# Performance work log

Hardware: AMD Instinct MI355X
Metric: run time of the kernel (lower is better)

The kernel has to match this reference:

```python
import jax, jax.numpy as jnp
import numpy as np

B = 16384
D_IN = 1024
D_OUT = 512
H1 = 4 * D_IN      # floor(layersDimentions[0]*inputDimention) = 4096
H3 = 4 * D_OUT     # floor(layersDimentions[1]*outputDimention) = 2048
H4 = 4 * D_OUT     # floor(layersDimentions[2]*outputDimention) = 2048
M = 256            # codebook size


def _linear_params(key, fan_in, fan_out):
    kw, kb = jax.random.split(key)
    bound = 1.0 / np.sqrt(fan_in)
    w = jax.random.uniform(kw, (fan_out, fan_in), jnp.float32, -bound, bound)
    b = jax.random.uniform(kb, (fan_out,), jnp.float32, -bound, bound)
    return w, b


def setup_inputs() -> dict:
    key = jax.random.key(0)
    ks = jax.random.split(key, 7)
    x = jax.random.normal(ks[0], (B, D_IN), jnp.float32)
    codebook = jnp.sort(jax.random.normal(ks[1], (M,), jnp.float32))
    w1, b1 = _linear_params(ks[2], D_IN, H1)
    w2, b2 = _linear_params(ks[3], H1, D_OUT)
    w3, b3 = _linear_params(ks[4], D_OUT, H3)
    w4, b4 = _linear_params(ks[5], H3, H4)
    w5, b5 = _linear_params(ks[6], H4, D_OUT)
    return {"x": x, "codebook": codebook,
            "w1": w1, "b1": b1, "w2": w2, "b2": b2,
            "w3": w3, "b3": b3, "w4": w4, "b4": b4,
            "w5": w5, "b5": b5}


def _quantize(x, codebook):
    # nearest codeword per scalar element: argmin_m |x - c_m|
    # x: [B, D], codebook: [M]
    d = jnp.abs(x[..., None] - codebook)          # [B, D, M]
    idx = jnp.argmin(d, axis=-1)                  # [B, D]
    return codebook[idx]


def reference(x, codebook, w1, b1, w2, b2, w3, b3, w4, b4, w5, b5):
    h = x @ w1.T + b1                # [B, H1]
    h = h @ w2.T + b2                # [B, D_OUT]
    h = _quantize(h, codebook)       # [B, D_OUT]
    h = h @ w3.T + b3                # [B, H3]
    h = h @ w4.T + b4                # [B, H4]
    return h @ w5.T + b5             # [B, D_OUT]
```

## Files before the change

### kernel.cpp

```cpp
#include <hip/hip_runtime.h>


typedef __bf16 v8bf __attribute__((ext_vector_type(8)));
typedef float  v4f  __attribute__((ext_vector_type(4)));

#define Bdim   16384
#define DIN    1024
#define DOUT   512
#define H1dim  4096
#define H3dim  2048
#define H4dim  2048

#define GLOBAL_AS __attribute__((address_space(1)))
#define LDS_AS    __attribute__((address_space(3)))

__device__ __forceinline__ void load16_to_lds(const __bf16* g, __bf16* l) {
  __builtin_amdgcn_global_load_lds((const GLOBAL_AS unsigned int*)g,
                                   (LDS_AS unsigned int*)l, 16, 0, 0);
}

__device__ __forceinline__ unsigned pack2bf(float a, float b) {
  return (unsigned)__builtin_bit_cast(unsigned short, (__bf16)a) |
         ((unsigned)__builtin_bit_cast(unsigned short, (__bf16)b) << 16);
}

__device__ __forceinline__ void transpose_body(const float* __restrict__ in,
                                               __bf16* __restrict__ out,
                                               int R, int C, int bx, int by,
                                               float (*tile)[68]) {
  const int c0 = bx * 32, r0 = by * 64;
  const int t = threadIdx.x, tr = t >> 5, tc = t & 31;
#pragma unroll
  for (int i = 0; i < 8; ++i)
    tile[tc][tr + i * 8] = in[(size_t)(r0 + tr + i * 8) * C + (c0 + tc)];
  __syncthreads();
  const int orow = t >> 3, oc = (t & 7) * 8;
  float4 a = *(const float4*)&tile[orow][oc];
  float4 b = *(const float4*)&tile[orow][oc + 4];
  int4 o;
  o.x = pack2bf(a.x, a.y); o.y = pack2bf(a.z, a.w);
  o.z = pack2bf(b.x, b.y); o.w = pack2bf(b.z, b.w);
  *(int4*)&out[(size_t)(c0 + orow) * R + (r0 + oc)] = o;
}

__device__ __forceinline__ void cast_body(const float* __restrict__ in,
                                          __bf16* __restrict__ out, int b) {
  const size_t i = (size_t)b * 2048 + (size_t)threadIdx.x * 8;
  float4 a = *(const float4*)&in[i];
  float4 c = *(const float4*)&in[i + 4];
  int4 o;
  o.x = pack2bf(a.x, a.y); o.y = pack2bf(a.z, a.w);
  o.z = pack2bf(c.x, c.y); o.w = pack2bf(c.z, c.w);
  *(int4*)&out[i] = o;
}

__global__ void prep_kernel(const float* __restrict__ w1, __bf16* __restrict__ w1T,
                            const float* __restrict__ w4, __bf16* __restrict__ w4T,
                            const float* __restrict__ w3, __bf16* __restrict__ w3T,
                            const float* __restrict__ x, __bf16* __restrict__ xb,
                            const float* __restrict__ w2, __bf16* __restrict__ w2b,
                            const float* __restrict__ w5, __bf16* __restrict__ w5b) {
  __shared__ float tile[32][68];
  int b = blockIdx.x;
  if (b < 2048) {
    transpose_body(w1, w1T, H1dim, DIN, b & 31, b >> 5, tile);
  } else if (b < 4096) {
    b -= 2048;
    transpose_body(w4, w4T, H4dim, H3dim, b & 63, b >> 6, tile);
  } else if (b < 4608) {
    b -= 4096;
    transpose_body(w3, w3T, H3dim, DOUT, b & 15, b >> 4, tile);
  } else if (b < 12800) {
    cast_body(x, xb, b - 4608);
  } else if (b < 13824) {
    cast_body(w2, w2b, b - 12800);
  } else {
    cast_body(w5, w5b, b - 13824);
  }
}

__device__ __forceinline__ void bias_ba_body(int bb, const float* __restrict__ b1,
                                             const float* __restrict__ w2,
                                             const float* __restrict__ b2,
                                             float* __restrict__ ba) {
  const int wave = threadIdx.x >> 6, lane = threadIdx.x & 63;
  const int j = bb * 4 + wave;
  float s = 0.f;
  for (int k = lane; k < H1dim; k += 64) s += b1[k] * w2[(size_t)j * H1dim + k];
#pragma unroll
  for (int off = 32; off; off >>= 1) s += __shfl_xor(s, off, 64);
  if (lane == 0) ba[j] = s + b2[j];
}

__device__ __forceinline__ void bias_bc_body(int bb, const float* __restrict__ b3,
                                             const __bf16* __restrict__ WtT,
                                             const float* __restrict__ b4,
                                             const float* __restrict__ w5,
                                             const float* __restrict__ b5,
                                             float* __restrict__ bc) {
  const int wave = threadIdx.x >> 6, lane = threadIdx.x & 63;
  const int j = bb * 4 + wave;
  float s = 0.f;
  for (int k = lane; k < H4dim; k += 64)
    s += b3[k] * (float)WtT[(size_t)j * H4dim + k] + b4[k] * w5[(size_t)j * H4dim + k];
#pragma unroll
  for (int off = 32; off; off >>= 1) s += __shfl_xor(s, off, 64);
  if (lane == 0) bc[j] = s + b5[j];
}

enum { MODE_W = 0, MODE_Q = 1, MODE_OUT = 2 };

#define ASM_BAR() asm volatile("s_barrier" ::: "memory")

template <int MODE, int BM>
__device__ __forceinline__ void gemm_body(__bf16* As, __bf16* Bs, float* cbs,
                                          int bx, int by,
                                          const __bf16* __restrict__ A,
                                          const __bf16* __restrict__ Bt,
                                          void* __restrict__ Cout,
                                          const float* __restrict__ bias,
                                          const float* __restrict__ codebook,
                                          int M, int N, int K, int CH) {
  const int t = threadIdx.x;
  const int m0 = bx * BM, n0 = by * 64;
  if constexpr (MODE == MODE_Q) cbs[t] = codebook[t];

  const int lane = t & 63, wave = t >> 6;
  const int quad = lane >> 4, l15 = lane & 15;
  constexpr int MI = BM / 32;
  const int wm = (wave & 1) * (BM / 2), wn = (wave >> 1) * 32;

  const int lrow = lane >> 3;
  const int gcol = ((lane & 7) ^ lrow) * 8;
  const __bf16* gA = A  + (size_t)(m0 + (BM / 4) * wave + lrow) * K + gcol;
  const __bf16* gB = Bt + (size_t)(n0 + 16 * wave + lrow) * K + gcol;
  const int swz = l15 & 7;

  v4f acc[MI][2], accT[MI][2];
#pragma unroll
  for (int i = 0; i < MI; ++i)
#pragma unroll
    for (int j = 0; j < 2; ++j) {
      acc[i][j] = (v4f){0.f, 0.f, 0.f, 0.f};
      if constexpr (MODE == MODE_W) accT[i][j] = (v4f){0.f, 0.f, 0.f, 0.f};
    }

  auto stage = [&](int k0, int buf) {
    __bf16* lA = As + buf * (BM * 64) + (BM / 4) * wave * 64;
    __bf16* lB = Bs + buf * (64 * 64) + 16 * wave * 64;
#pragma unroll
    for (int p = 0; p < MI; ++p)
      load16_to_lds(gA + (size_t)(8 * p) * K + k0, lA + p * 512);
#pragma unroll
    for (int p = 0; p < 2; ++p)
      load16_to_lds(gB + (size_t)(8 * p) * K + k0, lB + p * 512);
  };

  const int nk = K >> 6;
  const int chsteps = CH >> 6;
  stage(0, 0);
  stage(64, 1);

  int cc = 0;
  for (int tk = 0; tk < nk; ++tk) {
    if (tk + 1 < nk) {
      if constexpr (BM == 128) asm volatile("s_waitcnt vmcnt(6)" ::: "memory");
      else                     asm volatile("s_waitcnt vmcnt(4)" ::: "memory");
    } else {
      asm volatile("s_waitcnt vmcnt(0)" ::: "memory");
    }
    ASM_BAR();

    const __bf16* cA = As + (tk & 1) * (BM * 64);
    const __bf16* cB = Bs + (tk & 1) * (64 * 64);
#pragma unroll
    for (int kk = 0; kk < 2; ++kk) {
      const int cch = ((kk * 4 + quad) ^ swz) * 8;
      v8bf af[MI], bv[2];
#pragma unroll
      for (int i = 0; i < MI; ++i)
        af[i] = *(const v8bf*)&cA[(wm + i * 16 + l15) * 64 + cch];
#pragma unroll
      for (int j = 0; j < 2; ++j)
        bv[j] = *(const v8bf*)&cB[(wn + j * 16 + l15) * 64 + cch];
#pragma unroll
      for (int i = 0; i < MI; ++i)
#pragma unroll
        for (int j = 0; j < 2; ++j)
          acc[i][j] = __builtin_amdgcn_mfma_f32_16x16x32_bf16(af[i], bv[j], acc[i][j], 0, 0, 0);
    }
    if constexpr (MODE == MODE_W) {
      if (++cc == chsteps) {
        cc = 0;
#pragma unroll
        for (int i = 0; i < MI; ++i)
#pragma unroll
          for (int j = 0; j < 2; ++j) {
            accT[i][j] += acc[i][j];
            acc[i][j] = (v4f){0.f, 0.f, 0.f, 0.f};
          }
      }
    }
    asm volatile("s_waitcnt lgkmcnt(0)" ::: "memory");
    ASM_BAR();
    if (tk + 2 < nk) stage((tk + 2) << 6, tk & 1);
  }

#pragma unroll
  for (int j = 0; j < 2; ++j) {
    const int gn = n0 + wn + j * 16 + l15;
    float bj = 0.f;
    if constexpr (MODE != MODE_W) bj = bias[gn];
#pragma unroll
    for (int i = 0; i < MI; ++i) {
#pragma unroll
      for (int r = 0; r < 4; ++r) {
        const int gm = m0 + wm + i * 16 + quad * 4 + r;
        if constexpr (MODE == MODE_W) {
          ((__bf16*)Cout)[(size_t)gm * N + gn] = (__bf16)accT[i][j][r];
        } else if constexpr (MODE == MODE_Q) {
          float v = acc[i][j][r] + bj;
          int idx = 0;
#pragma unroll
          for (int s = 128; s > 0; s >>= 1) {
            const int u = idx + s;
            if (cbs[u] <= v) idx = u;
          }
          float best = cbs[idx];
          if (idx < 255) {
            const float c1 = cbs[idx + 1];
            if (!(v - best <= c1 - v)) best = c1;
          }
          ((__bf16*)Cout)[(size_t)gm * N + gn] = (__bf16)best;
        } else {
          ((float*)Cout)[(size_t)gm * N + gn] = acc[i][j][r] + bj;
        }
      }
    }
  }
}

__global__ __launch_bounds__(256, 3)
void foldA_kernel(const __bf16* __restrict__ w2b, const __bf16* __restrict__ w1T,
                  __bf16* __restrict__ WaT,
                  const __bf16* __restrict__ w5b, const __bf16* __restrict__ w4T,
                  __bf16* __restrict__ WtT,
                  const float* __restrict__ b1, const float* __restrict__ w2,
                  const float* __restrict__ b2, float* __restrict__ ba) {
  __shared__ __align__(16) __bf16 As[2 * 64 * 64];
  __shared__ __align__(16) __bf16 Bs[2 * 64 * 64];
  int b = blockIdx.x;
  if (b < 128) {
    const int c = b & 7, i = b >> 3;
    gemm_body<MODE_W, 64>(As, Bs, nullptr, i >> 1, c * 2 + (i & 1), w2b, w1T, WaT,
                          nullptr, nullptr, DOUT, DIN, H1dim, 512);
  } else if (b < 384) {
    b -= 128;
    const int c = b & 7, i = b >> 3;
    gemm_body<MODE_W, 64>(As, Bs, nullptr, i >> 2, c * 4 + (i & 3), w5b, w4T, WtT,
                          nullptr, nullptr, DOUT, H3dim, H4dim, 512);
  } else {
    bias_ba_body(b - 384, b1, w2, b2, ba);
  }
}

__global__ __launch_bounds__(256, 3)
void foldB_kernel(const __bf16* __restrict__ WtT, const __bf16* __restrict__ w3T,
                  __bf16* __restrict__ WcT,
                  const float* __restrict__ b3, const float* __restrict__ b4,
                  const float* __restrict__ w5, const float* __restrict__ b5,
                  float* __restrict__ bc,
                  const __bf16* __restrict__ xb, const __bf16* __restrict__ WaT,
                  __bf16* __restrict__ q, const float* __restrict__ ba,
                  const float* __restrict__ cb) {
  __shared__ __align__(16) __bf16 As[2 * 128 * 64];
  __shared__ __align__(16) __bf16 Bs[2 * 64 * 64];
  __shared__ float cbs[256];
  int b = blockIdx.x;
  if (b < 64) {
    const int c = b & 7, i = b >> 3;
    gemm_body<MODE_W, 64>(As, Bs, nullptr, i, c, WtT, w3T, WcT,
                          nullptr, nullptr, DOUT, DOUT, H3dim, 256);
  } else if (b < 192) {
    bias_bc_body(b - 64, b3, WtT, b4, w5, b5, bc);
  } else {
    b -= 192;
    const int c = b & 7, i = b >> 3;
    gemm_body<MODE_Q, 128>(As, Bs, cbs, c * 16 + (i >> 3), i & 7, xb, WaT, q,
                           ba, cb, Bdim, DOUT, DIN, DIN);
  }
}

__global__ __launch_bounds__(256, 3)
void gemmout_kernel(const __bf16* __restrict__ q, const __bf16* __restrict__ WcT,
                    float* __restrict__ out, const float* __restrict__ bc) {
  __shared__ __align__(16) __bf16 As[2 * 128 * 64];
  __shared__ __align__(16) __bf16 Bs[2 * 64 * 64];
  const int b = blockIdx.x;
  const int c = b & 7, i = b >> 3;
  gemm_body<MODE_OUT, 128>(As, Bs, nullptr, c * 16 + (i >> 3), i & 7,
                           q, WcT, out, bc, nullptr, Bdim, DOUT, DOUT, DOUT);
}

extern "C" void kernel_launch(void* const* d_in, const int* in_sizes, int n_in,
                              void* d_out, int out_size, void* d_ws, size_t ws_size,
                              hipStream_t stream) {
  const float* x  = (const float*)d_in[0];
  const float* cb = (const float*)d_in[1];
  const float* w1 = (const float*)d_in[2];
  const float* b1 = (const float*)d_in[3];
  const float* w2 = (const float*)d_in[4];
  const float* b2 = (const float*)d_in[5];
  const float* w3 = (const float*)d_in[6];
  const float* b3 = (const float*)d_in[7];
  const float* w4 = (const float*)d_in[8];
  const float* b4 = (const float*)d_in[9];
  const float* w5 = (const float*)d_in[10];
  const float* b5 = (const float*)d_in[11];
  float* out = (float*)d_out;

  char* ws = (char*)d_ws;
  size_t off = 0;
  auto alloc = [&](size_t bytes) -> void* {
    void* p = ws + off;
    off = (off + bytes + 255) & ~(size_t)255;
    return p;
  };
  __bf16* w1T = (__bf16*)alloc((size_t)DIN * H1dim * 2);
  __bf16* w4T = (__bf16*)alloc((size_t)H3dim * H4dim * 2);
  __bf16* w3T = (__bf16*)alloc((size_t)DOUT * H3dim * 2);
  __bf16* w2b = (__bf16*)alloc((size_t)DOUT * H1dim * 2);
  __bf16* w5b = (__bf16*)alloc((size_t)DOUT * H4dim * 2);
  __bf16* WaT = (__bf16*)alloc((size_t)DOUT * DIN * 2);
  __bf16* WtT = (__bf16*)alloc((size_t)DOUT * H3dim * 2);
  __bf16* WcT = (__bf16*)alloc((size_t)DOUT * DOUT * 2);
  __bf16* q   = (__bf16*)alloc((size_t)Bdim * DOUT * 2);
  __bf16* xb  = (__bf16*)alloc((size_t)Bdim * DIN * 2);
  float*  ba  = (float*)alloc(DOUT * 4);
  float*  bc  = (float*)alloc(DOUT * 4);

  prep_kernel<<<14336, 256, 0, stream>>>(w1, w1T, w4, w4T, w3, w3T,
                                         x, xb, w2, w2b, w5, w5b);

  foldA_kernel<<<512, 256, 0, stream>>>(w2b, w1T, WaT, w5b, w4T, WtT,
                                        b1, w2, b2, ba);

  foldB_kernel<<<1216, 256, 0, stream>>>(WtT, w3T, WcT, b3, b4, w5, b5, bc,
                                         xb, WaT, q, ba, cb);

  gemmout_kernel<<<1024, 256, 0, stream>>>(q, WcT, out, bc);
}
```

Before: 268.0 us.

## Fuse quantize GEMM and output GEMM into one kernel with LDS-resident q tile

Replaces the separate quantize-GEMM (x·Wa + codebook snap) and output GEMM with a single kernel. Each block computes a 64-row by 512-column tile, quantizes it into shared memory, then multiplies it by WcT directly, so the q intermediate never goes to global memory. The fold work for WcT and bc moves into its own small kernel, because it can no longer share a launch with the q GEMM. In exchange the fused kernel launches only 256 blocks at one block per CU with a large LDS footprint. It also holds 64 accumulator vectors per thread and reloads WcT for every block without double-buffering in the second phase, which risks lower occupancy and poorer latency hiding.

```diff
diff --git a/kernel.cpp b/kernel.cpp
--- a/kernel.cpp
+++ b/kernel.cpp
@@ -108,23 +108,19 @@
   if (lane == 0) bc[j] = s + b5[j];
 }
 
-enum { MODE_W = 0, MODE_Q = 1, MODE_OUT = 2 };
+enum { MODE_W = 0 };
 
 #define ASM_BAR() asm volatile("s_barrier" ::: "memory")
 
 template <int MODE, int BM>
-__device__ __forceinline__ void gemm_body(__bf16* As, __bf16* Bs, float* cbs,
+__device__ __forceinline__ void gemm_body(__bf16* As, __bf16* Bs,
                                           int bx, int by,
                                           const __bf16* __restrict__ A,
                                           const __bf16* __restrict__ Bt,
                                           void* __restrict__ Cout,
-                                          const float* __restrict__ bias,
-                                          const float* __restrict__ codebook,
                                           int M, int N, int K, int CH) {
   const int t = threadIdx.x;
   const int m0 = bx * BM, n0 = by * 64;
-  if constexpr (MODE == MODE_Q) cbs[t] = codebook[t];
-
   const int lane = t & 63, wave = t >> 6;
   const int quad = lane >> 4, l15 = lane & 15;
   constexpr int MI = BM / 32;
@@ -142,7 +138,7 @@
 #pragma unroll
     for (int j = 0; j < 2; ++j) {
       acc[i][j] = (v4f){0.f, 0.f, 0.f, 0.f};
-      if constexpr (MODE == MODE_W) accT[i][j] = (v4f){0.f, 0.f, 0.f, 0.f};
+      accT[i][j] = (v4f){0.f, 0.f, 0.f, 0.f};
     }
 
   auto stage = [&](int k0, int buf) {
@@ -163,12 +159,8 @@
 
   int cc = 0;
   for (int tk = 0; tk < nk; ++tk) {
-    if (tk + 1 < nk) {
-      if constexpr (BM == 128) asm volatile("s_waitcnt vmcnt(6)" ::: "memory");
-      else                     asm volatile("s_waitcnt vmcnt(4)" ::: "memory");
-    } else {
-      asm volatile("s_waitcnt vmcnt(0)" ::: "memory");
-    }
+    if (tk + 1 < nk) asm volatile("s_waitcnt vmcnt(4)" ::: "memory");
+    else             asm volatile("s_waitcnt vmcnt(0)" ::: "memory");
     ASM_BAR();
 
     const __bf16* cA = As + (tk & 1) * (BM * 64);
@@ -189,17 +181,15 @@
         for (int j = 0; j < 2; ++j)
           acc[i][j] = __builtin_amdgcn_mfma_f32_16x16x32_bf16(af[i], bv[j], acc[i][j], 0, 0, 0);
     }
-    if constexpr (MODE == MODE_W) {
-      if (++cc == chsteps) {
-        cc = 0;
-#pragma unroll
-        for (int i = 0; i < MI; ++i)
-#pragma unroll
-          for (int j = 0; j < 2; ++j) {
-            accT[i][j] += acc[i][j];
-            acc[i][j] = (v4f){0.f, 0.f, 0.f, 0.f};
-          }
-      }
+    if (++cc == chsteps) {
+      cc = 0;
+#pragma unroll
+      for (int i = 0; i < MI; ++i)
+#pragma unroll
+        for (int j = 0; j < 2; ++j) {
+          accT[i][j] += acc[i][j];
+          acc[i][j] = (v4f){0.f, 0.f, 0.f, 0.f};
+        }
     }
     asm volatile("s_waitcnt lgkmcnt(0)" ::: "memory");
     ASM_BAR();
@@ -209,34 +199,13 @@
 #pragma unroll
   for (int j = 0; j < 2; ++j) {
     const int gn = n0 + wn + j * 16 + l15;
-    float bj = 0.f;
-    if constexpr (MODE != MODE_W) bj = bias[gn];
-#pragma unroll
-    for (int i = 0; i < MI; ++i) {
-#pragma unroll
-      for (int r = 0; r < 4; ++r) {
-        const int gm = m0 + wm + i * 16 + quad * 4 + r;
-        if constexpr (MODE == MODE_W) {
-          ((__bf16*)Cout)[(size_t)gm * N + gn] = (__bf16)accT[i][j][r];
-        } else if constexpr (MODE == MODE_Q) {
-          float v = acc[i][j][r] + bj;
-          int idx = 0;
-#pragma unroll
-          for (int s = 128; s > 0; s >>= 1) {
-            const int u = idx + s;
-            if (cbs[u] <= v) idx = u;
-          }
-          float best = cbs[idx];
-          if (idx < 255) {
-            const float c1 = cbs[idx + 1];
-            if (!(v - best <= c1 - v)) best = c1;
-          }
-          ((__bf16*)Cout)[(size_t)gm * N + gn] = (__bf16)best;
-        } else {
-          ((float*)Cout)[(size_t)gm * N + gn] = acc[i][j][r] + bj;
-        }
+#pragma unroll
+    for (int i = 0; i < MI; ++i)
+#pragma unroll
+      for (int r2 = 0; r2 < 4; ++r2) {
+        const int gm = m0 + wm + i * 16 + quad * 4 + r2;
+        ((__bf16*)Cout)[(size_t)gm * N + gn] = (__bf16)accT[i][j][r2];
       }
-    }
   }
 }
 
@@ -252,54 +221,177 @@
   int b = blockIdx.x;
   if (b < 128) {
     const int c = b & 7, i = b >> 3;
-    gemm_body<MODE_W, 64>(As, Bs, nullptr, i >> 1, c * 2 + (i & 1), w2b, w1T, WaT,
-                          nullptr, nullptr, DOUT, DIN, H1dim, 512);
+    gemm_body<MODE_W, 64>(As, Bs, i >> 1, c * 2 + (i & 1), w2b, w1T, WaT,
+                          DOUT, DIN, H1dim, 512);
   } else if (b < 384) {
     b -= 128;
     const int c = b & 7, i = b >> 3;
-    gemm_body<MODE_W, 64>(As, Bs, nullptr, i >> 2, c * 4 + (i & 3), w5b, w4T, WtT,
-                          nullptr, nullptr, DOUT, H3dim, H4dim, 512);
+    gemm_body<MODE_W, 64>(As, Bs, i >> 2, c * 4 + (i & 3), w5b, w4T, WtT,
+                          DOUT, H3dim, H4dim, 512);
   } else {
     bias_ba_body(b - 384, b1, w2, b2, ba);
   }
 }
 
 __global__ __launch_bounds__(256, 3)
-void foldB_kernel(const __bf16* __restrict__ WtT, const __bf16* __restrict__ w3T,
-                  __bf16* __restrict__ WcT,
-                  const float* __restrict__ b3, const float* __restrict__ b4,
-                  const float* __restrict__ w5, const float* __restrict__ b5,
-                  float* __restrict__ bc,
-                  const __bf16* __restrict__ xb, const __bf16* __restrict__ WaT,
-                  __bf16* __restrict__ q, const float* __restrict__ ba,
-                  const float* __restrict__ cb) {
-  __shared__ __align__(16) __bf16 As[2 * 128 * 64];
+void foldB2_kernel(const __bf16* __restrict__ WtT, const __bf16* __restrict__ w3T,
+                   __bf16* __restrict__ WcT,
+                   const float* __restrict__ b3, const float* __restrict__ b4,
+                   const float* __restrict__ w5, const float* __restrict__ b5,
+                   float* __restrict__ bc) {
+  __shared__ __align__(16) __bf16 As[2 * 64 * 64];
   __shared__ __align__(16) __bf16 Bs[2 * 64 * 64];
-  __shared__ float cbs[256];
   int b = blockIdx.x;
   if (b < 64) {
     const int c = b & 7, i = b >> 3;
-    gemm_body<MODE_W, 64>(As, Bs, nullptr, i, c, WtT, w3T, WcT,
-                          nullptr, nullptr, DOUT, DOUT, H3dim, 256);
-  } else if (b < 192) {
+    gemm_body<MODE_W, 64>(As, Bs, i, c, WtT, w3T, WcT, DOUT, DOUT, H3dim, 256);
+  } else {
     bias_bc_body(b - 64, b3, WtT, b4, w5, b5, bc);
-  } else {
-    b -= 192;
-    const int c = b & 7, i = b >> 3;
-    gemm_body<MODE_Q, 128>(As, Bs, cbs, c * 16 + (i >> 3), i & 7, xb, WaT, q,
-                           ba, cb, Bdim, DOUT, DIN, DIN);
-  }
-}
-
-__global__ __launch_bounds__(256, 3)
-void gemmout_kernel(const __bf16* __restrict__ q, const __bf16* __restrict__ WcT,
-                    float* __restrict__ out, const float* __restrict__ bc) {
-  __shared__ __align__(16) __bf16 As[2 * 128 * 64];
-  __shared__ __align__(16) __bf16 Bs[2 * 64 * 64];
-  const int b = blockIdx.x;
-  const int c = b & 7, i = b >> 3;
-  gemm_body<MODE_OUT, 128>(As, Bs, nullptr, c * 16 + (i >> 3), i & 7,
-                           q, WcT, out, bc, nullptr, Bdim, DOUT, DOUT, DOUT);
+  }
+}
+
+__global__ __launch_bounds__(256, 1)
+void fused_qo_kernel(const __bf16* __restrict__ xb, const __bf16* __restrict__ WaT,
+                     const __bf16* __restrict__ WcT,
+                     const float* __restrict__ ba, const float* __restrict__ bc,
+                     const float* __restrict__ cb, float* __restrict__ out) {
+  __shared__ __align__(16) __bf16 qs[64 * 512];
+  __shared__ __align__(16) __bf16 Bb[2 * 512 * 32];
+  __shared__ __align__(16) __bf16 Ab[2 * 64 * 32];
+  __shared__ float cbs[256];
+
+  const int t = threadIdx.x, lane = t & 63, wave = t >> 6;
+  const int quad = lane >> 4, l15 = lane & 15;
+  const int m0 = blockIdx.x * 64;
+  cbs[t] = cb[t];
+
+  const int wm = (wave & 1) * 32, wn = (wave >> 1) * 32;
+
+  const int scol = ((lane & 3) ^ ((lane >> 3) & 3)) * 8;
+  const __bf16* gA = xb  + (size_t)(m0 + 16 * wave + (lane >> 2)) * 1024 + scol;
+  const __bf16* gB = WaT + (size_t)(128 * wave + (lane >> 2)) * 1024 + scol;
+
+  auto stage1 = [&](int k0, int buf) {
+    load16_to_lds(gA + k0, Ab + buf * 2048 + wave * 512);
+#pragma unroll
+    for (int p = 0; p < 8; ++p)
+      load16_to_lds(gB + (size_t)p * 16384 + k0, Bb + buf * 16384 + wave * 4096 + p * 512);
+  };
+
+  v4f acc[8][2][2];
+#pragma unroll
+  for (int jn = 0; jn < 8; ++jn)
+#pragma unroll
+    for (int i = 0; i < 2; ++i)
+#pragma unroll
+      for (int j = 0; j < 2; ++j) acc[jn][i][j] = (v4f){0.f, 0.f, 0.f, 0.f};
+
+  stage1(0, 0);
+  stage1(32, 1);
+
+  const int rk = (l15 >> 1) & 3;
+  for (int ks = 0; ks < 32; ++ks) {
+    if (ks + 1 < 32) asm volatile("s_waitcnt vmcnt(9)" ::: "memory");
+    else             asm volatile("s_waitcnt vmcnt(0)" ::: "memory");
+    ASM_BAR();
+
+    const __bf16* cA = Ab + (ks & 1) * 2048;
+    const __bf16* cB = Bb + (ks & 1) * 16384;
+    const int cch = (quad ^ rk) * 8;
+    v8bf af0 = *(const v8bf*)&cA[(wm +  0 + l15) * 32 + cch];
+    v8bf af1 = *(const v8bf*)&cA[(wm + 16 + l15) * 32 + cch];
+#pragma unroll
+    for (int jn = 0; jn < 8; ++jn) {
+      v8bf bv0 = *(const v8bf*)&cB[(jn * 64 + wn +  0 + l15) * 32 + cch];
+      v8bf bv1 = *(const v8bf*)&cB[(jn * 64 + wn + 16 + l15) * 32 + cch];
+      acc[jn][0][0] = __builtin_amdgcn_mfma_f32_16x16x32_bf16(af0, bv0, acc[jn][0][0], 0, 0, 0);
+      acc[jn][1][0] = __builtin_amdgcn_mfma_f32_16x16x32_bf16(af1, bv0, acc[jn][1][0], 0, 0, 0);
+      acc[jn][0][1] = __builtin_amdgcn_mfma_f32_16x16x32_bf16(af0, bv1, acc[jn][0][1], 0, 0, 0);
+      acc[jn][1][1] = __builtin_amdgcn_mfma_f32_16x16x32_bf16(af1, bv1, acc[jn][1][1], 0, 0, 0);
+    }
+    asm volatile("s_waitcnt lgkmcnt(0)" ::: "memory");
+    ASM_BAR();
+    if (ks + 2 < 32) stage1((ks + 2) * 32, ks & 1);
+  }
+
+#pragma unroll
+  for (int jn = 0; jn < 8; ++jn) {
+#pragma unroll
+    for (int j = 0; j < 2; ++j) {
+      const int cc = wn + j * 16 + l15;
+      const float bj = ba[jn * 64 + cc];
+#pragma unroll
+      for (int i = 0; i < 2; ++i) {
+#pragma unroll
+        for (int r = 0; r < 4; ++r) {
+          const int row = wm + i * 16 + quad * 4 + r;
+          float v = acc[jn][i][j][r] + bj;
+          int idx = 0;
+#pragma unroll
+          for (int s = 128; s > 0; s >>= 1) {
+            const int u = idx + s;
+            if (cbs[u] <= v) idx = u;
+          }
+          float best = cbs[idx];
+          if (idx < 255) {
+            const float c1 = cbs[idx + 1];
+            if (!(v - best <= c1 - v)) best = c1;
+          }
+          qs[row * 512 + jn * 64 + (((cc >> 3) ^ (row & 7)) * 8) + (cc & 7)] = (__bf16)best;
+        }
+      }
+    }
+  }
+  asm volatile("s_waitcnt lgkmcnt(0)" ::: "memory");
+  ASM_BAR();
+
+#pragma unroll 1
+  for (int jn2 = 0; jn2 < 8; ++jn2) {
+    const int n02 = jn2 * 64;
+#pragma unroll
+    for (int p = 0; p < 16; ++p) {
+      const int row = 16 * wave + p;
+      const int g = (lane >> 3) * 64 + (((lane & 7) ^ (p & 7)) * 8);
+      load16_to_lds(WcT + (size_t)(n02 + row) * 512 + g, Bb + row * 512);
+    }
+    asm volatile("s_waitcnt vmcnt(0)" ::: "memory");
+    ASM_BAR();
+
+    v4f a2[2][2];
+#pragma unroll
+    for (int i = 0; i < 2; ++i)
+#pragma unroll
+      for (int j = 0; j < 2; ++j) a2[i][j] = (v4f){0.f, 0.f, 0.f, 0.f};
+
+#pragma unroll
+    for (int kt = 0; kt < 8; ++kt) {
+#pragma unroll
+      for (int kk = 0; kk < 2; ++kk) {
+        const int pos = (((kk * 4 + quad) ^ (l15 & 7)) * 8);
+        v8bf af0 = *(const v8bf*)&qs[(wm +  0 + l15) * 512 + kt * 64 + pos];
+        v8bf af1 = *(const v8bf*)&qs[(wm + 16 + l15) * 512 + kt * 64 + pos];
+        v8bf bv0 = *(const v8bf*)&Bb[(wn +  0 + l15) * 512 + kt * 64 + pos];
+        v8bf bv1 = *(const v8bf*)&Bb[(wn + 16 + l15) * 512 + kt * 64 + pos];
+        a2[0][0] = __builtin_amdgcn_mfma_f32_16x16x32_bf16(af0, bv0, a2[0][0], 0, 0, 0);
+        a2[1][0] = __builtin_amdgcn_mfma_f32_16x16x32_bf16(af1, bv0, a2[1][0], 0, 0, 0);
+        a2[0][1] = __builtin_amdgcn_mfma_f32_16x16x32_bf16(af0, bv1, a2[0][1], 0, 0, 0);
+        a2[1][1] = __builtin_amdgcn_mfma_f32_16x16x32_bf16(af1, bv1, a2[1][1], 0, 0, 0);
+      }
+    }
+
+#pragma unroll
+    for (int j = 0; j < 2; ++j) {
+      const int gn = n02 + wn + j * 16 + l15;
+      const float bj = bc[gn];
+#pragma unroll
+      for (int i = 0; i < 2; ++i)
+#pragma unroll
+        for (int r = 0; r < 4; ++r)
+          out[(size_t)(m0 + wm + i * 16 + quad * 4 + r) * 512 + gn] = a2[i][j][r] + bj;
+    }
+    asm volatile("s_waitcnt lgkmcnt(0)" ::: "memory");
+    ASM_BAR();
+  }
 }
 
 extern "C" void kernel_launch(void* const* d_in, const int* in_sizes, int n_in,
@@ -334,7 +426,6 @@
   __bf16* WaT = (__bf16*)alloc((size_t)DOUT * DIN * 2);
   __bf16* WtT = (__bf16*)alloc((size_t)DOUT * H3dim * 2);
   __bf16* WcT = (__bf16*)alloc((size_t)DOUT * DOUT * 2);
-  __bf16* q   = (__bf16*)alloc((size_t)Bdim * DOUT * 2);
   __bf16* xb  = (__bf16*)alloc((size_t)Bdim * DIN * 2);
   float*  ba  = (float*)alloc(DOUT * 4);
   float*  bc  = (float*)alloc(DOUT * 4);
@@ -345,8 +436,7 @@
   foldA_kernel<<<512, 256, 0, stream>>>(w2b, w1T, WaT, w5b, w4T, WtT,
                                         b1, w2, b2, ba);
 
-  foldB_kernel<<<1216, 256, 0, stream>>>(WtT, w3T, WcT, b3, b4, w5, b5, bc,
-                                         xb, WaT, q, ba, cb);
-
-  gemmout_kernel<<<1024, 256, 0, stream>>>(q, WcT, out, bc);
-}
+  foldB2_kernel<<<192, 256, 0, stream>>>(WtT, w3T, WcT, b3, b4, w5, b5, bc);
+
+  fused_qo_kernel<<<256, 256, 0, stream>>>(xb, WaT, WcT, ba, bc, cb, out);
+}
```

After: 354.0 us. +32.1%, slower.
